# Optimization experiments

Measured on AMD Instinct MI355X. Metric: run time of the kernel, lower is better.

Reference implementation:

```python
import jax, jax.numpy as jnp
import numpy as np

N = 50000
E = 800000
D = 128
L = 3
BN_EPS = 1e-5


def _bn(h, gamma, beta, mean, var):
    # eval-mode BatchNorm1d using running stats
    return (h - mean) * (gamma * jax.lax.rsqrt(var + BN_EPS)) + beta


def setup_inputs() -> dict:
    key = jax.random.key(0)
    ks = jax.random.split(key, 8)
    x = jax.random.normal(ks[0], (N, D), dtype=jnp.float32)
    edge_index = jax.random.randint(ks[1], (2, E), 0, N, dtype=jnp.int32)
    s = 1.0 / np.sqrt(D)
    W1 = jax.random.uniform(ks[2], (L, D, D), jnp.float32, -s, s)
    b1 = jax.random.uniform(ks[3], (L, D), jnp.float32, -s, s)
    W2 = jax.random.uniform(ks[4], (L, D, D), jnp.float32, -s, s)
    b2 = jax.random.uniform(ks[5], (L, D), jnp.float32, -s, s)
    # BN params: [L, 2, D] -> (inner mlp BN, outer BN) gamma/beta; running mean/var
    g = jnp.ones((L, 2, D), jnp.float32)
    be = jnp.zeros((L, 2, D), jnp.float32)
    rm = jax.random.normal(ks[6], (L, 2, D), dtype=jnp.float32) * 0.1
    rv = jax.random.uniform(ks[7], (L, 2, D), jnp.float32, 0.5, 1.5)
    return {"x": x, "edge_index": edge_index, "W1": W1, "b1": b1, "W2": W2,
            "b2": b2, "g": g, "be": be, "rm": rm, "rv": rv}


def reference(x, edge_index, W1, b1, W2, b2, g, be, rm, rv):
    src, dst = edge_index[0], edge_index[1]
    h = x
    for i in range(L):
        # GINConv (eps=0): (1+eps)*h + sum over in-neighbors
        agg = jax.ops.segment_sum(h[src], dst, num_segments=N)
        h = h + agg
        # mlp: Linear -> BN -> ReLU -> Linear
        h = jnp.maximum(_bn(h @ W1[i] + b1[i], g[i, 0], be[i, 0], rm[i, 0], rv[i, 0]), 0.0)
        h = h @ W2[i] + b2[i]
        # outer BN + ReLU (dropout is identity in eval)
        h = jnp.maximum(_bn(h, g[i, 1], be[i, 1], rm[i, 1], rv[i, 1]), 0.0)
    return h
```

## Files before the change

kernel.cpp:

```cpp
#include <hip/hip_runtime.h>
#include <stdint.h>

#define NN 50000
#define NE 800000
#define DD 128
#define NL 3
#define NB_E 200
#define EPB 4000
#define NBK 196
#define MH (NBK*NB_E)
#define LSTR 136

typedef __attribute__((ext_vector_type(8))) short short8;
typedef __attribute__((ext_vector_type(4))) float f32x4;

__device__ __forceinline__ float b2f(unsigned short u){
  union { unsigned int i; float f; } v; v.i = ((unsigned int)u) << 16; return v.f;
}
__device__ __forceinline__ unsigned short f2b(float f){
  union { float f; unsigned int i; } v; v.f = f;
  unsigned int r = 0x7FFFu + ((v.i >> 16) & 1u);
  return (unsigned short)((v.i + r) >> 16);
}

__global__ __launch_bounds__(256) void k_hist(const int* __restrict__ dst,
                                              int* __restrict__ blkhist){
  __shared__ int h[NBK];
  int t = threadIdx.x, b = blockIdx.x;
  for (int i = t; i < NBK; i += 256) h[i] = 0;
  __syncthreads();
  int e0 = b * EPB;
  for (int i = t; i < EPB; i += 256){
    int d = dst[e0 + i];
    atomicAdd(&h[d >> 8], 1);
  }
  __syncthreads();
  for (int i = t; i < NBK; i += 256) blkhist[i * NB_E + b] = h[i];
}

__global__ void k_scanA(const int* __restrict__ in, int* __restrict__ out,
                        int* __restrict__ bsum, int n){
  __shared__ int s[256];
  int t = threadIdx.x, i = blockIdx.x * 256 + t;
  int v = (i < n) ? in[i] : 0;
  s[t] = v; __syncthreads();
  for (int d = 1; d < 256; d <<= 1){
    int x = (t >= d) ? s[t - d] : 0;
    __syncthreads();
    s[t] += x;
    __syncthreads();
  }
  if (i < n) out[i] = s[t] - v;
  if (t == 255) bsum[blockIdx.x] = s[255];
}

__global__ void k_scanB(int* __restrict__ bsum, int nblk){
  __shared__ int s[256];
  int t = threadIdx.x;
  int v = (t < nblk) ? bsum[t] : 0;
  s[t] = v; __syncthreads();
  for (int d = 1; d < 256; d <<= 1){
    int x = (t >= d) ? s[t - d] : 0;
    __syncthreads();
    s[t] += x;
    __syncthreads();
  }
  if (t < nblk) bsum[t] = s[t] - v;
}

__global__ void k_scanC(int* __restrict__ out, const int* __restrict__ bsum, int n){
  int i = blockIdx.x * 256 + threadIdx.x;
  if (i < n) out[i] += bsum[blockIdx.x];
}

__global__ __launch_bounds__(256) void k_bin(const int* __restrict__ src,
    const int* __restrict__ dst, const int* __restrict__ pos,
    unsigned int* __restrict__ binned){
  __shared__ int cur[NBK];
  int t = threadIdx.x, b = blockIdx.x;
  for (int i = t; i < NBK; i += 256) cur[i] = pos[i * NB_E + b];
  __syncthreads();
  int e0 = b * EPB;
  for (int i = t; i < EPB; i += 256){
    int d = dst[e0 + i];
    int s = src[e0 + i];
    int p = atomicAdd(&cur[d >> 8], 1);
    binned[p] = ((unsigned int)d << 16) | (unsigned int)s;
  }
}

__global__ __launch_bounds__(256) void k_csr(const unsigned int* __restrict__ binned,
    const int* __restrict__ pos, int* __restrict__ offs, int* __restrict__ counts,
    int* __restrict__ csr_src){
  __shared__ int h[256], ex[256], cur[256];
  int t = threadIdx.x, b = blockIdx.x;
  int r0 = pos[b * NB_E];
  int r1 = (b == NBK - 1) ? NE : pos[(b + 1) * NB_E];
  h[t] = 0; __syncthreads();
  for (int i = r0 + t; i < r1; i += 256){
    unsigned int pv = binned[i];
    atomicAdd(&h[(pv >> 16) & 255], 1);
  }
  __syncthreads();
  int v = h[t];
  ex[t] = v; __syncthreads();
  for (int d = 1; d < 256; d <<= 1){
    int x = (t >= d) ? ex[t - d] : 0;
    __syncthreads();
    ex[t] += x;
    __syncthreads();
  }
  int base = r0 + ex[t] - v;
  cur[t] = base;
  int gd = b * 256 + t;
  if (gd < NN){ offs[gd] = base; counts[gd] = v; }
  __syncthreads();
  for (int i = r0 + t; i < r1; i += 256){
    unsigned int pv = binned[i];
    int dl = (pv >> 16) & 255;
    int s = pv & 0xFFFF;
    int p = atomicAdd(&cur[dl], 1);
    csr_src[p] = s;
  }
}

__global__ void k_prep_w(const float* __restrict__ W1, const float* __restrict__ W2,
    unsigned short* __restrict__ Wthi, unsigned short* __restrict__ Wtlo){
  int idx = blockIdx.x * 256 + threadIdx.x;
  int mat = idx >> 14;
  int rem = idx & 16383;
  int k = rem >> 7, j = rem & 127;
  int layer = mat >> 1, which = mat & 1;
  const float* srcW = which ? W2 : W1;
  float w = srcW[layer * 16384 + k * DD + j];
  unsigned short hi = f2b(w);
  Wthi[mat * 16384 + j * DD + k] = hi;
  Wtlo[mat * 16384 + j * DD + k] = f2b(w - b2f(hi));
}

__global__ void k_prep_bn(const float* __restrict__ b1, const float* __restrict__ b2,
    const float* __restrict__ g, const float* __restrict__ be,
    const float* __restrict__ rm, const float* __restrict__ rv,
    float* __restrict__ sc, float* __restrict__ sh){
  int idx = blockIdx.x * 256 + threadIdx.x;
  if (idx >= NL * 2 * DD) return;
  int j = idx & 127;
  int w = (idx >> 7) & 1;
  int l = idx >> 8;
  int p = (l * 2 + w) * DD + j;
  float s = g[p] * rsqrtf(rv[p] + 1e-5f);
  float bias = w ? b2[l * DD + j] : b1[l * DD + j];
  sc[p] = s;
  sh[p] = fmaf(bias - rm[p], s, be[p]);
}

__global__ void k_cvt(const float* __restrict__ x,
    unsigned short* __restrict__ hi, unsigned short* __restrict__ lo){
  int i = blockIdx.x * 256 + threadIdx.x;
  float4 a = ((const float4*)x)[2 * i];
  float4 b = ((const float4*)x)[2 * i + 1];
  float v[8] = {a.x, a.y, a.z, a.w, b.x, b.y, b.z, b.w};
  short8 h8, l8;
  #pragma unroll
  for (int c = 0; c < 8; ++c){
    unsigned short h = f2b(v[c]);
    h8[c] = (short)h; l8[c] = (short)f2b(v[c] - b2f(h));
  }
  ((short8*)hi)[i] = h8;
  ((short8*)lo)[i] = l8;
}

__global__ __launch_bounds__(256, 8) void k_agg(
    const unsigned short* __restrict__ Shi, const unsigned short* __restrict__ Slo,
    const int* __restrict__ offs, const int* __restrict__ counts,
    const int* __restrict__ csr_src,
    unsigned short* __restrict__ Ahi, unsigned short* __restrict__ Alo){
  int t = blockIdx.x * 256 + threadIdx.x;
  int row = t >> 4;
  int l = t & 15;
  const short8* H = (const short8*)Shi;
  const short8* L = (const short8*)Slo;
  int idx = row * 16 + l;
  short8 s_h = H[idx]; short8 s_l = L[idx];
  float acc[8];
  #pragma unroll
  for (int i = 0; i < 8; ++i)
    acc[i] = b2f((unsigned short)s_h[i]) + b2f((unsigned short)s_l[i]);

  int e = offs[row];
  int end = e + counts[row];
  for (; e + 8 <= end; e += 8){
    int i0 = csr_src[e],   i1 = csr_src[e+1], i2 = csr_src[e+2], i3 = csr_src[e+3];
    int i4 = csr_src[e+4], i5 = csr_src[e+5], i6 = csr_src[e+6], i7 = csr_src[e+7];
    short8 g0 = H[i0*16+l], g1 = H[i1*16+l], g2 = H[i2*16+l], g3 = H[i3*16+l];
    short8 g4 = H[i4*16+l], g5 = H[i5*16+l], g6 = H[i6*16+l], g7 = H[i7*16+l];
    #pragma unroll
    for (int i = 0; i < 8; ++i){
      acc[i] += (b2f((unsigned short)g0[i]) + b2f((unsigned short)g1[i]))
              + (b2f((unsigned short)g2[i]) + b2f((unsigned short)g3[i]))
              + (b2f((unsigned short)g4[i]) + b2f((unsigned short)g5[i]))
              + (b2f((unsigned short)g6[i]) + b2f((unsigned short)g7[i]));
    }
  }
  for (; e < end; ++e){
    short8 g0 = H[csr_src[e]*16 + l];
    #pragma unroll
    for (int i = 0; i < 8; ++i) acc[i] += b2f((unsigned short)g0[i]);
  }

  short8 oh, ol;
  #pragma unroll
  for (int i = 0; i < 8; ++i){
    unsigned short h = f2b(acc[i]);
    oh[i] = (short)h; ol[i] = (short)f2b(acc[i] - b2f(h));
  }
  ((short8*)Ahi)[idx] = oh;
  ((short8*)Alo)[idx] = ol;
}

template<int LAST>
__global__ __launch_bounds__(128, 2) void k_mlp3(
    const unsigned short* __restrict__ Ahi, const unsigned short* __restrict__ Alo,
    const unsigned short* __restrict__ W1h, const unsigned short* __restrict__ W1l,
    const unsigned short* __restrict__ W2h, const unsigned short* __restrict__ W2l,
    const float* __restrict__ sc1, const float* __restrict__ sh1,
    const float* __restrict__ sc2, const float* __restrict__ sh2,
    unsigned short* __restrict__ Ohi, unsigned short* __restrict__ Olo,
    float* __restrict__ Of)
{
  __shared__ __align__(16) char smem[2 * 64 * LSTR * 2];
  unsigned short* Hhi_s = (unsigned short*)smem;
  unsigned short* Hlo_s = Hhi_s + 64 * LSTR;

  int t = threadIdx.x;
  int base = blockIdx.x * 64;
  int wave = t >> 6, lane = t & 63, l16 = lane & 15, q = lane >> 4;
  int c0 = wave * 64;

  const short8* AH = (const short8*)Ahi;
  const short8* AL = (const short8*)Alo;
  const short8* B1H = (const short8*)W1h;
  const short8* B1L = (const short8*)W1l;
  const short8* B2H = (const short8*)W2h;
  const short8* B2L = (const short8*)W2l;

  int ar[4];
  #pragma unroll
  for (int rt = 0; rt < 4; ++rt){
    int r = base + rt * 16 + l16;
    ar[rt] = (r > NN - 1) ? (NN - 1) : r;
  }

  f32x4 acc[4][4];
  #pragma unroll
  for (int rt = 0; rt < 4; ++rt)
    #pragma unroll
    for (int ct = 0; ct < 4; ++ct) acc[rt][ct] = (f32x4){0.f, 0.f, 0.f, 0.f};

  #pragma unroll
  for (int kc = 0; kc < 4; ++kc){
    short8 ah[4], al[4], bh[4], bl[4];
    #pragma unroll
    for (int rt = 0; rt < 4; ++rt){
      ah[rt] = AH[ar[rt] * 16 + kc * 4 + q];
      al[rt] = AL[ar[rt] * 16 + kc * 4 + q];
    }
    #pragma unroll
    for (int ct = 0; ct < 4; ++ct){
      int wr = c0 + ct * 16 + l16;
      bh[ct] = B1H[wr * 16 + kc * 4 + q];
      bl[ct] = B1L[wr * 16 + kc * 4 + q];
    }
    #pragma unroll
    for (int rt = 0; rt < 4; ++rt)
      #pragma unroll
      for (int ct = 0; ct < 4; ++ct){
        acc[rt][ct] = __builtin_amdgcn_mfma_f32_16x16x32_bf16(ah[rt], bh[ct], acc[rt][ct], 0, 0, 0);
        acc[rt][ct] = __builtin_amdgcn_mfma_f32_16x16x32_bf16(ah[rt], bl[ct], acc[rt][ct], 0, 0, 0);
        acc[rt][ct] = __builtin_amdgcn_mfma_f32_16x16x32_bf16(al[rt], bh[ct], acc[rt][ct], 0, 0, 0);
      }
  }

  #pragma unroll
  for (int ct = 0; ct < 4; ++ct){
    int col = c0 + ct * 16 + l16;
    float s = sc1[col], b = sh1[col];
    #pragma unroll
    for (int rt = 0; rt < 4; ++rt)
      #pragma unroll
      for (int r = 0; r < 4; ++r){
        int rl = rt * 16 + q * 4 + r;
        float v = fmaxf(fmaf(acc[rt][ct][r], s, b), 0.f);
        unsigned short h = f2b(v);
        Hhi_s[rl * LSTR + col] = h;
        Hlo_s[rl * LSTR + col] = f2b(v - b2f(h));
      }
  }
  __syncthreads();

  f32x4 acc2[4][4];
  #pragma unroll
  for (int rt = 0; rt < 4; ++rt)
    #pragma unroll
    for (int ct = 0; ct < 4; ++ct) acc2[rt][ct] = (f32x4){0.f, 0.f, 0.f, 0.f};

  #pragma unroll
  for (int kc = 0; kc < 4; ++kc){
    short8 ah[4], al[4], bh[4], bl[4];
    #pragma unroll
    for (int rt = 0; rt < 4; ++rt){
      ah[rt] = *(const short8*)&Hhi_s[(rt * 16 + l16) * LSTR + kc * 32 + q * 8];
      al[rt] = *(const short8*)&Hlo_s[(rt * 16 + l16) * LSTR + kc * 32 + q * 8];
    }
    #pragma unroll
    for (int ct = 0; ct < 4; ++ct){
      int wr = c0 + ct * 16 + l16;
      bh[ct] = B2H[wr * 16 + kc * 4 + q];
      bl[ct] = B2L[wr * 16 + kc * 4 + q];
    }
    #pragma unroll
    for (int rt = 0; rt < 4; ++rt)
      #pragma unroll
      for (int ct = 0; ct < 4; ++ct){
        acc2[rt][ct] = __builtin_amdgcn_mfma_f32_16x16x32_bf16(ah[rt], bh[ct], acc2[rt][ct], 0, 0, 0);
        acc2[rt][ct] = __builtin_amdgcn_mfma_f32_16x16x32_bf16(ah[rt], bl[ct], acc2[rt][ct], 0, 0, 0);
        acc2[rt][ct] = __builtin_amdgcn_mfma_f32_16x16x32_bf16(al[rt], bh[ct], acc2[rt][ct], 0, 0, 0);
      }
  }
  __syncthreads();

  if (!LAST){
    #pragma unroll
    for (int ct = 0; ct < 4; ++ct){
      int col = c0 + ct * 16 + l16;
      float s = sc2[col], b = sh2[col];
      #pragma unroll
      for (int rt = 0; rt < 4; ++rt)
        #pragma unroll
        for (int r = 0; r < 4; ++r){
          int rl = rt * 16 + q * 4 + r;
          float v = fmaxf(fmaf(acc2[rt][ct][r], s, b), 0.f);
          unsigned short h = f2b(v);
          Hhi_s[rl * LSTR + col] = h;
          Hlo_s[rl * LSTR + col] = f2b(v - b2f(h));
        }
    }
    int rr = lane >> 3, ch = lane & 7;
    #pragma unroll
    for (int i = 0; i < 8; ++i){
      int rl = i * 8 + rr;
      int rg = base + rl;
      short8 vh = *(const short8*)&Hhi_s[rl * LSTR + c0 + ch * 8];
      short8 vl = *(const short8*)&Hlo_s[rl * LSTR + c0 + ch * 8];
      if (rg < NN){
        *(short8*)&Ohi[rg * DD + c0 + ch * 8] = vh;
        *(short8*)&Olo[rg * DD + c0 + ch * 8] = vl;
      }
    }
  } else {
    float* Cf = (float*)smem;
    #pragma unroll
    for (int ct = 0; ct < 4; ++ct){
      int col = c0 + ct * 16 + l16;
      float s = sc2[col], b = sh2[col];
      #pragma unroll
      for (int rt = 0; rt < 4; ++rt)
        #pragma unroll
        for (int r = 0; r < 4; ++r){
          int rl = rt * 16 + q * 4 + r;
          Cf[rl * 132 + col] = fmaxf(fmaf(acc2[rt][ct][r], s, b), 0.f);
        }
    }
    int rr = lane >> 4, cf = (lane & 15) * 4;
    #pragma unroll
    for (int i = 0; i < 16; ++i){
      int rl = i * 4 + rr;
      int rg = base + rl;
      float4 v = *(const float4*)&Cf[rl * 132 + c0 + cf];
      if (rg < NN) *(float4*)&Of[rg * DD + c0 + cf] = v;
    }
  }
}

extern "C" void kernel_launch(void* const* d_in, const int* in_sizes, int n_in,
                              void* d_out, int out_size, void* d_ws, size_t ws_size,
                              hipStream_t stream) {
  const float* x  = (const float*)d_in[0];
  const int* ei   = (const int*)d_in[1];
  const float* W1 = (const float*)d_in[2];
  const float* b1 = (const float*)d_in[3];
  const float* W2 = (const float*)d_in[4];
  const float* b2 = (const float*)d_in[5];
  const float* g  = (const float*)d_in[6];
  const float* be = (const float*)d_in[7];
  const float* rm = (const float*)d_in[8];
  const float* rv = (const float*)d_in[9];

  const int* src = ei;
  const int* dst = ei + NE;

  char* w = (char*)d_ws;
  const size_t HB = (size_t)NN * DD * sizeof(unsigned short);
  unsigned short* S0hi = (unsigned short*)w; w += HB;
  unsigned short* S0lo = (unsigned short*)w; w += HB;
  unsigned short* S1hi = (unsigned short*)w; w += HB;
  unsigned short* S1lo = (unsigned short*)w; w += HB;
  unsigned short* Ahi  = (unsigned short*)w; w += HB;
  unsigned short* Alo  = (unsigned short*)w; w += HB;
  unsigned short* Wthi = (unsigned short*)w; w += 6 * 16384 * sizeof(unsigned short);
  unsigned short* Wtlo = (unsigned short*)w; w += 6 * 16384 * sizeof(unsigned short);
  float* scv = (float*)w; w += NL * 2 * DD * sizeof(float);
  float* shv = (float*)w; w += NL * 2 * DD * sizeof(float);
  int* counts  = (int*)w; w += 200192;
  int* offs    = (int*)w; w += 200192;
  int* blkhist = (int*)w; w += MH * sizeof(int);
  int* pos     = (int*)w; w += MH * sizeof(int);
  int* bsum    = (int*)w; w += 1024;
  unsigned int* binned = (unsigned int*)w; w += (size_t)NE * sizeof(unsigned int);
  int* csr_src = (int*)w; w += (size_t)NE * sizeof(int);

  const int SCAN_BLK = (MH + 255) / 256;
  k_hist<<<NB_E, 256, 0, stream>>>(dst, blkhist);
  k_scanA<<<SCAN_BLK, 256, 0, stream>>>(blkhist, pos, bsum, MH);
  k_scanB<<<1, 256, 0, stream>>>(bsum, SCAN_BLK);
  k_scanC<<<SCAN_BLK, 256, 0, stream>>>(pos, bsum, MH);
  k_bin<<<NB_E, 256, 0, stream>>>(src, dst, pos, binned);
  k_csr<<<NBK, 256, 0, stream>>>(binned, pos, offs, counts, csr_src);

  k_prep_w<<<384, 256, 0, stream>>>(W1, W2, Wthi, Wtlo);
  k_prep_bn<<<3, 256, 0, stream>>>(b1, b2, g, be, rm, rv, scv, shv);
  k_cvt<<<NN * DD / 8 / 256, 256, 0, stream>>>(x, S0hi, S0lo);

  const int AGG_BLOCKS = NN * 16 / 256;
  const int MLP_BLOCKS = (NN + 63) / 64;

  for (int i = 0; i < NL; ++i){
    const unsigned short* W1h = Wthi + (size_t)(i * 2 + 0) * 16384;
    const unsigned short* W1l = Wtlo + (size_t)(i * 2 + 0) * 16384;
    const unsigned short* W2h = Wthi + (size_t)(i * 2 + 1) * 16384;
    const unsigned short* W2l = Wtlo + (size_t)(i * 2 + 1) * 16384;
    const float* sc1 = scv + (size_t)(i * 2 + 0) * DD;
    const float* sh1 = shv + (size_t)(i * 2 + 0) * DD;
    const float* sc2 = scv + (size_t)(i * 2 + 1) * DD;
    const float* sh2 = shv + (size_t)(i * 2 + 1) * DD;

    const unsigned short* Ih = (i & 1) ? S1hi : S0hi;
    const unsigned short* Il = (i & 1) ? S1lo : S0lo;
    unsigned short* Oh = (i & 1) ? S0hi : S1hi;
    unsigned short* Ol = (i & 1) ? S0lo : S1lo;

    k_agg<<<AGG_BLOCKS, 256, 0, stream>>>(Ih, Il, offs, counts, csr_src, Ahi, Alo);

    if (i == NL - 1){
      k_mlp3<1><<<MLP_BLOCKS, 128, 0, stream>>>(Ahi, Alo,
          W1h, W1l, W2h, W2l, sc1, sh1, sc2, sh2,
          (unsigned short*)nullptr, (unsigned short*)nullptr, (float*)d_out);
    } else {
      k_mlp3<0><<<MLP_BLOCKS, 128, 0, stream>>>(Ahi, Alo,
          W1h, W1l, W2h, W2l, sc1, sh1, sc2, sh2, Oh, Ol, (float*)nullptr);
    }
  }
}
```

Measured before the change: 319.6 us.

## Merge scan and prep kernels, halve MLP row tile to 32

Replaces the three-kernel multi-block scan with a single 1024-thread block that scans 39 entries per thread serially. It also fuses the weight split, BN folding and input bf16 conversion into one prep kernel. The MLP kernel now processes 32 rows per block instead of 64, with launch bounds raised to 4 blocks per CU, to improve occupancy and tail balance. The aims are fewer launches and better latency hiding. In exchange the single-block scan is serial per thread, and each MLP block reloads the weight tiles for fewer rows.

```diff
diff --git a/kernel.cpp b/kernel.cpp
--- a/kernel.cpp
+++ b/kernel.cpp
@@ -38,39 +38,32 @@
   for (int i = t; i < NBK; i += 256) blkhist[i * NB_E + b] = h[i];
 }
 
-__global__ void k_scanA(const int* __restrict__ in, int* __restrict__ out,
-                        int* __restrict__ bsum, int n){
-  __shared__ int s[256];
-  int t = threadIdx.x, i = blockIdx.x * 256 + t;
-  int v = (i < n) ? in[i] : 0;
-  s[t] = v; __syncthreads();
-  for (int d = 1; d < 256; d <<= 1){
+__global__ __launch_bounds__(1024) void k_scan1k(const int* __restrict__ in,
+                                                 int* __restrict__ out){
+  __shared__ int s[1024];
+  int t = threadIdx.x;
+  int b0 = t * 39;
+  int sum = 0;
+  for (int i = 0; i < 39; ++i){
+    int ix = b0 + i;
+    sum += (ix < MH) ? in[ix] : 0;
+  }
+  s[t] = sum; __syncthreads();
+  for (int d = 1; d < 1024; d <<= 1){
     int x = (t >= d) ? s[t - d] : 0;
     __syncthreads();
     s[t] += x;
     __syncthreads();
   }
-  if (i < n) out[i] = s[t] - v;
-  if (t == 255) bsum[blockIdx.x] = s[255];
-}
-
-__global__ void k_scanB(int* __restrict__ bsum, int nblk){
-  __shared__ int s[256];
-  int t = threadIdx.x;
-  int v = (t < nblk) ? bsum[t] : 0;
-  s[t] = v; __syncthreads();
-  for (int d = 1; d < 256; d <<= 1){
-    int x = (t >= d) ? s[t - d] : 0;
-    __syncthreads();
-    s[t] += x;
-    __syncthreads();
-  }
-  if (t < nblk) bsum[t] = s[t] - v;
-}
-
-__global__ void k_scanC(int* __restrict__ out, const int* __restrict__ bsum, int n){
-  int i = blockIdx.x * 256 + threadIdx.x;
-  if (i < n) out[i] += bsum[blockIdx.x];
+  int run = s[t] - sum;
+  for (int i = 0; i < 39; ++i){
+    int ix = b0 + i;
+    if (ix < MH){
+      int v = in[ix];
+      out[ix] = run;
+      run += v;
+    }
+  }
 }
 
 __global__ __launch_bounds__(256) void k_bin(const int* __restrict__ src,
@@ -124,50 +117,49 @@
   }
 }
 
-__global__ void k_prep_w(const float* __restrict__ W1, const float* __restrict__ W2,
-    unsigned short* __restrict__ Wthi, unsigned short* __restrict__ Wtlo){
-  int idx = blockIdx.x * 256 + threadIdx.x;
-  int mat = idx >> 14;
-  int rem = idx & 16383;
-  int k = rem >> 7, j = rem & 127;
-  int layer = mat >> 1, which = mat & 1;
-  const float* srcW = which ? W2 : W1;
-  float w = srcW[layer * 16384 + k * DD + j];
-  unsigned short hi = f2b(w);
-  Wthi[mat * 16384 + j * DD + k] = hi;
-  Wtlo[mat * 16384 + j * DD + k] = f2b(w - b2f(hi));
-}
-
-__global__ void k_prep_bn(const float* __restrict__ b1, const float* __restrict__ b2,
+__global__ __launch_bounds__(256) void k_prep(const float* __restrict__ x,
+    const float* __restrict__ W1, const float* __restrict__ W2,
+    const float* __restrict__ b1, const float* __restrict__ b2,
     const float* __restrict__ g, const float* __restrict__ be,
     const float* __restrict__ rm, const float* __restrict__ rv,
+    unsigned short* __restrict__ Shi, unsigned short* __restrict__ Slo,
+    unsigned short* __restrict__ Wthi, unsigned short* __restrict__ Wtlo,
     float* __restrict__ sc, float* __restrict__ sh){
   int idx = blockIdx.x * 256 + threadIdx.x;
-  if (idx >= NL * 2 * DD) return;
-  int j = idx & 127;
-  int w = (idx >> 7) & 1;
-  int l = idx >> 8;
-  int p = (l * 2 + w) * DD + j;
-  float s = g[p] * rsqrtf(rv[p] + 1e-5f);
-  float bias = w ? b2[l * DD + j] : b1[l * DD + j];
-  sc[p] = s;
-  sh[p] = fmaf(bias - rm[p], s, be[p]);
-}
-
-__global__ void k_cvt(const float* __restrict__ x,
-    unsigned short* __restrict__ hi, unsigned short* __restrict__ lo){
-  int i = blockIdx.x * 256 + threadIdx.x;
-  float4 a = ((const float4*)x)[2 * i];
-  float4 b = ((const float4*)x)[2 * i + 1];
-  float v[8] = {a.x, a.y, a.z, a.w, b.x, b.y, b.z, b.w};
-  short8 h8, l8;
-  #pragma unroll
-  for (int c = 0; c < 8; ++c){
-    unsigned short h = f2b(v[c]);
-    h8[c] = (short)h; l8[c] = (short)f2b(v[c] - b2f(h));
-  }
-  ((short8*)hi)[i] = h8;
-  ((short8*)lo)[i] = l8;
+  {
+    float4 a = ((const float4*)x)[2 * idx];
+    float4 b = ((const float4*)x)[2 * idx + 1];
+    float v[8] = {a.x, a.y, a.z, a.w, b.x, b.y, b.z, b.w};
+    short8 h8, l8;
+    #pragma unroll
+    for (int c = 0; c < 8; ++c){
+      unsigned short h = f2b(v[c]);
+      h8[c] = (short)h; l8[c] = (short)f2b(v[c] - b2f(h));
+    }
+    ((short8*)Shi)[idx] = h8;
+    ((short8*)Slo)[idx] = l8;
+  }
+  if (idx < 6 * DD * DD){
+    int mat = idx >> 14;
+    int rem = idx & 16383;
+    int k = rem >> 7, j = rem & 127;
+    int layer = mat >> 1, which = mat & 1;
+    const float* srcW = which ? W2 : W1;
+    float w = srcW[layer * 16384 + k * DD + j];
+    unsigned short hi = f2b(w);
+    Wthi[mat * 16384 + j * DD + k] = hi;
+    Wtlo[mat * 16384 + j * DD + k] = f2b(w - b2f(hi));
+  }
+  if (idx < NL * 2 * DD){
+    int j = idx & 127;
+    int w2 = (idx >> 7) & 1;
+    int l = idx >> 8;
+    int p = (l * 2 + w2) * DD + j;
+    float s = g[p] * rsqrtf(rv[p] + 1e-5f);
+    float bias = w2 ? b2[l * DD + j] : b1[l * DD + j];
+    sc[p] = s;
+    sh[p] = fmaf(bias - rm[p], s, be[p]);
+  }
 }
 
 __global__ __launch_bounds__(256, 8) void k_agg(
@@ -219,7 +211,7 @@
 }
 
 template<int LAST>
-__global__ __launch_bounds__(128, 2) void k_mlp3(
+__global__ __launch_bounds__(128, 4) void k_mlp(
     const unsigned short* __restrict__ Ahi, const unsigned short* __restrict__ Alo,
     const unsigned short* __restrict__ W1h, const unsigned short* __restrict__ W1l,
     const unsigned short* __restrict__ W2h, const unsigned short* __restrict__ W2l,
@@ -228,12 +220,12 @@
     unsigned short* __restrict__ Ohi, unsigned short* __restrict__ Olo,
     float* __restrict__ Of)
 {
-  __shared__ __align__(16) char smem[2 * 64 * LSTR * 2];
+  __shared__ __align__(16) char smem[2 * 32 * LSTR * 2];
   unsigned short* Hhi_s = (unsigned short*)smem;
-  unsigned short* Hlo_s = Hhi_s + 64 * LSTR;
+  unsigned short* Hlo_s = Hhi_s + 32 * LSTR;
 
   int t = threadIdx.x;
-  int base = blockIdx.x * 64;
+  int base = blockIdx.x * 32;
   int wave = t >> 6, lane = t & 63, l16 = lane & 15, q = lane >> 4;
   int c0 = wave * 64;
 
@@ -244,24 +236,24 @@
   const short8* B2H = (const short8*)W2h;
   const short8* B2L = (const short8*)W2l;
 
-  int ar[4];
-  #pragma unroll
-  for (int rt = 0; rt < 4; ++rt){
+  int ar[2];
+  #pragma unroll
+  for (int rt = 0; rt < 2; ++rt){
     int r = base + rt * 16 + l16;
     ar[rt] = (r > NN - 1) ? (NN - 1) : r;
   }
 
-  f32x4 acc[4][4];
-  #pragma unroll
-  for (int rt = 0; rt < 4; ++rt)
+  f32x4 acc[2][4];
+  #pragma unroll
+  for (int rt = 0; rt < 2; ++rt)
     #pragma unroll
     for (int ct = 0; ct < 4; ++ct) acc[rt][ct] = (f32x4){0.f, 0.f, 0.f, 0.f};
 
   #pragma unroll
   for (int kc = 0; kc < 4; ++kc){
-    short8 ah[4], al[4], bh[4], bl[4];
-    #pragma unroll
-    for (int rt = 0; rt < 4; ++rt){
+    short8 ah[2], al[2], bh[4], bl[4];
+    #pragma unroll
+    for (int rt = 0; rt < 2; ++rt){
       ah[rt] = AH[ar[rt] * 16 + kc * 4 + q];
       al[rt] = AL[ar[rt] * 16 + kc * 4 + q];
     }
@@ -272,7 +264,7 @@
       bl[ct] = B1L[wr * 16 + kc * 4 + q];
     }
     #pragma unroll
-    for (int rt = 0; rt < 4; ++rt)
+    for (int rt = 0; rt < 2; ++rt)
       #pragma unroll
       for (int ct = 0; ct < 4; ++ct){
         acc[rt][ct] = __builtin_amdgcn_mfma_f32_16x16x32_bf16(ah[rt], bh[ct], acc[rt][ct], 0, 0, 0);
@@ -286,7 +278,7 @@
     int col = c0 + ct * 16 + l16;
     float s = sc1[col], b = sh1[col];
     #pragma unroll
-    for (int rt = 0; rt < 4; ++rt)
+    for (int rt = 0; rt < 2; ++rt)
       #pragma unroll
       for (int r = 0; r < 4; ++r){
         int rl = rt * 16 + q * 4 + r;
@@ -298,17 +290,17 @@
   }
   __syncthreads();
 
-  f32x4 acc2[4][4];
-  #pragma unroll
-  for (int rt = 0; rt < 4; ++rt)
+  f32x4 acc2[2][4];
+  #pragma unroll
+  for (int rt = 0; rt < 2; ++rt)
     #pragma unroll
     for (int ct = 0; ct < 4; ++ct) acc2[rt][ct] = (f32x4){0.f, 0.f, 0.f, 0.f};
 
   #pragma unroll
   for (int kc = 0; kc < 4; ++kc){
-    short8 ah[4], al[4], bh[4], bl[4];
-    #pragma unroll
-    for (int rt = 0; rt < 4; ++rt){
+    short8 ah[2], al[2], bh[4], bl[4];
+    #pragma unroll
+    for (int rt = 0; rt < 2; ++rt){
       ah[rt] = *(const short8*)&Hhi_s[(rt * 16 + l16) * LSTR + kc * 32 + q * 8];
       al[rt] = *(const short8*)&Hlo_s[(rt * 16 + l16) * LSTR + kc * 32 + q * 8];
     }
@@ -319,7 +311,7 @@
       bl[ct] = B2L[wr * 16 + kc * 4 + q];
     }
     #pragma unroll
-    for (int rt = 0; rt < 4; ++rt)
+    for (int rt = 0; rt < 2; ++rt)
       #pragma unroll
       for (int ct = 0; ct < 4; ++ct){
         acc2[rt][ct] = __builtin_amdgcn_mfma_f32_16x16x32_bf16(ah[rt], bh[ct], acc2[rt][ct], 0, 0, 0);
@@ -335,7 +327,7 @@
       int col = c0 + ct * 16 + l16;
       float s = sc2[col], b = sh2[col];
       #pragma unroll
-      for (int rt = 0; rt < 4; ++rt)
+      for (int rt = 0; rt < 2; ++rt)
         #pragma unroll
         for (int r = 0; r < 4; ++r){
           int rl = rt * 16 + q * 4 + r;
@@ -347,7 +339,7 @@
     }
     int rr = lane >> 3, ch = lane & 7;
     #pragma unroll
-    for (int i = 0; i < 8; ++i){
+    for (int i = 0; i < 4; ++i){
       int rl = i * 8 + rr;
       int rg = base + rl;
       short8 vh = *(const short8*)&Hhi_s[rl * LSTR + c0 + ch * 8];
@@ -364,7 +356,7 @@
       int col = c0 + ct * 16 + l16;
       float s = sc2[col], b = sh2[col];
       #pragma unroll
-      for (int rt = 0; rt < 4; ++rt)
+      for (int rt = 0; rt < 2; ++rt)
         #pragma unroll
         for (int r = 0; r < 4; ++r){
           int rl = rt * 16 + q * 4 + r;
@@ -373,7 +365,7 @@
     }
     int rr = lane >> 4, cf = (lane & 15) * 4;
     #pragma unroll
-    for (int i = 0; i < 16; ++i){
+    for (int i = 0; i < 8; ++i){
       int rl = i * 4 + rr;
       int rg = base + rl;
       float4 v = *(const float4*)&Cf[rl * 132 + c0 + cf];
@@ -415,24 +407,19 @@
   int* offs    = (int*)w; w += 200192;
   int* blkhist = (int*)w; w += MH * sizeof(int);
   int* pos     = (int*)w; w += MH * sizeof(int);
-  int* bsum    = (int*)w; w += 1024;
   unsigned int* binned = (unsigned int*)w; w += (size_t)NE * sizeof(unsigned int);
   int* csr_src = (int*)w; w += (size_t)NE * sizeof(int);
 
-  const int SCAN_BLK = (MH + 255) / 256;
   k_hist<<<NB_E, 256, 0, stream>>>(dst, blkhist);
-  k_scanA<<<SCAN_BLK, 256, 0, stream>>>(blkhist, pos, bsum, MH);
-  k_scanB<<<1, 256, 0, stream>>>(bsum, SCAN_BLK);
-  k_scanC<<<SCAN_BLK, 256, 0, stream>>>(pos, bsum, MH);
+  k_scan1k<<<1, 1024, 0, stream>>>(blkhist, pos);
   k_bin<<<NB_E, 256, 0, stream>>>(src, dst, pos, binned);
   k_csr<<<NBK, 256, 0, stream>>>(binned, pos, offs, counts, csr_src);
 
-  k_prep_w<<<384, 256, 0, stream>>>(W1, W2, Wthi, Wtlo);
-  k_prep_bn<<<3, 256, 0, stream>>>(b1, b2, g, be, rm, rv, scv, shv);
-  k_cvt<<<NN * DD / 8 / 256, 256, 0, stream>>>(x, S0hi, S0lo);
+  k_prep<<<NN * DD / 8 / 256, 256, 0, stream>>>(x, W1, W2, b1, b2, g, be, rm, rv,
+      S0hi, S0lo, Wthi, Wtlo, scv, shv);
 
   const int AGG_BLOCKS = NN * 16 / 256;
-  const int MLP_BLOCKS = (NN + 63) / 64;
+  const int MLP_BLOCKS = (NN + 31) / 32;
 
   for (int i = 0; i < NL; ++i){
     const unsigned short* W1h = Wthi + (size_t)(i * 2 + 0) * 16384;
@@ -452,11 +439,11 @@
     k_agg<<<AGG_BLOCKS, 256, 0, stream>>>(Ih, Il, offs, counts, csr_src, Ahi, Alo);
 
     if (i == NL - 1){
-      k_mlp3<1><<<MLP_BLOCKS, 128, 0, stream>>>(Ahi, Alo,
+      k_mlp<1><<<MLP_BLOCKS, 128, 0, stream>>>(Ahi, Alo,
           W1h, W1l, W2h, W2l, sc1, sh1, sc2, sh2,
           (unsigned short*)nullptr, (unsigned short*)nullptr, (float*)d_out);
     } else {
-      k_mlp3<0><<<MLP_BLOCKS, 128, 0, stream>>>(Ahi, Alo,
+      k_mlp<0><<<MLP_BLOCKS, 128, 0, stream>>>(Ahi, Alo,
           W1h, W1l, W2h, W2l, sc1, sh1, sc2, sh2, Oh, Ol, (float*)nullptr);
     }
   }
```

Measured after the change: 399.5 us. 1.25x slower.
